# Optimization experiments

Hardware: AMD Instinct MI355X
Metric: run time of the kernel (lower is better)

## Reference

```python
import jax, jax.numpy as jnp
import numpy as np

N_NODES = 100000
N_EDGES = 640000
IN_CH = 128
OUT_CH = 64
HID = 2 * OUT_CH


def setup_inputs() -> dict:
    key = jax.random.key(0)
    k1, k2, k3, k4, k5, k6 = jax.random.split(key, 6)
    x = jax.random.normal(k1, (N_NODES, IN_CH), dtype=jnp.float32)
    edge_index = jax.random.randint(k2, (2, N_EDGES), 0, N_NODES, dtype=jnp.int64)
    # GCNConv params (PyG: glorot weights, zero bias; random values fine for a numeric reference)
    W1 = jax.random.normal(k3, (IN_CH, HID), dtype=jnp.float32) / np.sqrt(IN_CH)
    b1 = jax.random.normal(k4, (HID,), dtype=jnp.float32) * 0.01
    W2 = jax.random.normal(k5, (HID, OUT_CH), dtype=jnp.float32) / np.sqrt(HID)
    b2 = jax.random.normal(k6, (OUT_CH,), dtype=jnp.float32) * 0.01
    return {"x": x, "edge_index": edge_index, "W1": W1, "b1": b1, "W2": W2, "b2": b2}


def _gcn_conv(x, row, col, norm, W, b, n_nodes):
    # PyG GCNConv: h = x @ W; out[col] += norm * h[row]; out += b
    h = x @ W  # [N, F_out]
    msg = h[row] * norm[:, None]  # gather + scale, [E+N, F_out]
    out = jax.ops.segment_sum(msg, col, num_segments=n_nodes)  # scatter-add
    return out + b


def reference(x, edge_index, W1, b1, W2, b2):
    n_nodes = x.shape[0]
    # add self-loops (PyG default add_self_loops=True)
    loop = jnp.arange(n_nodes, dtype=edge_index.dtype)
    row = jnp.concatenate([edge_index[0], loop])  # sources
    col = jnp.concatenate([edge_index[1], loop])  # targets (aggregation index)
    # symmetric normalization: deg over targets with unit edge weights
    deg = jax.ops.segment_sum(jnp.ones_like(col, dtype=x.dtype), col, num_segments=n_nodes)
    dinv = jnp.where(deg > 0, jax.lax.rsqrt(deg), 0.0)
    norm = dinv[row] * dinv[col]  # [E+N]
    h = jax.nn.relu(_gcn_conv(x, row, col, norm, W1, b1, n_nodes))
    return _gcn_conv(h, row, col, norm, W2, b2, n_nodes)
```

## Files before the change

kernel.cpp:

```cpp
#include <hip/hip_runtime.h>

namespace {
constexpr int N_NODES = 100000;
constexpr int N_EDGES = 640000;
constexpr int ROWTILES = N_NODES / 16;
constexpr int FILLBLK = N_EDGES / 1024;
constexpr int GEMM1BLK = (ROWTILES + 3) / 4;
constexpr int UGRID = 7 * 313;
constexpr int CAP = 16;
constexpr int SPILL_CAP = 65536;
}

typedef short bf16x8 __attribute__((ext_vector_type(8)));
typedef float f32x4 __attribute__((ext_vector_type(4)));

static __device__ inline uint32_t cvt_pk_bf16(float a, float b) {
  uint32_t r;
  asm volatile("v_cvt_pk_bf16_f32 %0, %1, %2" : "=v"(r) : "v"(a), "v"(b));
  return r;
}

static __device__ inline void bf8_to_f32(uint4 u, float* v) {
  v[0] = __uint_as_float(u.x << 16);
  v[1] = __uint_as_float(u.x & 0xffff0000u);
  v[2] = __uint_as_float(u.y << 16);
  v[3] = __uint_as_float(u.y & 0xffff0000u);
  v[4] = __uint_as_float(u.z << 16);
  v[5] = __uint_as_float(u.z & 0xffff0000u);
  v[6] = __uint_as_float(u.w << 16);
  v[7] = __uint_as_float(u.w & 0xffff0000u);
}

static __device__ inline uint4 f32_to_bf8(const float* v) {
  uint4 o;
  o.x = cvt_pk_bf16(v[0], v[1]);
  o.y = cvt_pk_bf16(v[2], v[3]);
  o.z = cvt_pk_bf16(v[4], v[5]);
  o.w = cvt_pk_bf16(v[6], v[7]);
  return o;
}


static __device__ inline void wpack(const float* __restrict__ W, int kout, int idx,
                                    uint4* __restrict__ wfrag) {
  int nt_cnt = kout / 16;
  int lane = idx & 63;
  int nt = (idx >> 6) % nt_cnt;
  int ks = idx / (64 * nt_cnt);
  int g = lane >> 4, c = lane & 15;
  const float* wp = W + (ks * 32 + g * 8) * kout + nt * 16 + c;
  float w[8];
#pragma unroll
  for (int j = 0; j < 8; ++j) w[j] = wp[j * kout];
  wfrag[idx] = f32_to_bf8(w);
}

__global__ void k_wprep_zero(const float* __restrict__ W1, const float* __restrict__ W2,
                             uint4* __restrict__ wf1, uint4* __restrict__ wf2,
                             int* __restrict__ deg_zero_base) {
  int idx = blockIdx.x * 256 + threadIdx.x;
  if (idx < 2048) {
    wpack(W1, 128, idx, wf1);
  } else if (idx < 3072) {
    wpack(W2, 64, idx - 2048, wf2);
  }
  int z = idx - 3072;
  if (z >= 0 && z < N_NODES + 16) deg_zero_base[z] = 0;
}


__global__ __launch_bounds__(256) void k_histfill_gemm1(
    const int* __restrict__ erow, const int* __restrict__ ecol,
    int* __restrict__ deg, int* __restrict__ csr16, int* __restrict__ nspill,
    int2* __restrict__ spill, const float* __restrict__ X,
    const uint4* __restrict__ wfrag, unsigned short* __restrict__ Yb) {
  const int tid = threadIdx.x;
  const int group = blockIdx.x / 7;
  const int pos = blockIdx.x % 7;

  if (pos < 2) {
    const int fb = group * 2 + pos;
    if (fb >= FILLBLK) return;
    const int e4 = fb * 256 + tid;
    int4 r4 = *(const int4*)&erow[e4 * 4];
    int4 c4 = *(const int4*)&ecol[e4 * 4];
    int rs[4] = {r4.x, r4.y, r4.z, r4.w};
    int cs[4] = {c4.x, c4.y, c4.z, c4.w};
#pragma unroll
    for (int k = 0; k < 4; ++k) {
      int p = atomicAdd(&deg[cs[k]], 1);
      if (p < CAP) {
        __builtin_nontemporal_store(rs[k], &csr16[cs[k] * CAP + p]);
      } else {
        int si = atomicAdd(nspill, 1);
        if (si < SPILL_CAP) {
          __builtin_nontemporal_store(rs[k], &spill[si].x);
          __builtin_nontemporal_store(cs[k], &spill[si].y);
        }
      }
    }
    return;
  }

  const int gb = group * 5 + (pos - 2);
  if (gb >= GEMM1BLK) return;
  const int wv = gb * 4 + (tid >> 6);
  if (wv >= ROWTILES) return;
  const int lane = tid & 63;
  const int g = lane >> 4, c = lane & 15;
  const int rb = wv * 16;

  constexpr int NT = 8;
  f32x4 acc[NT];
#pragma unroll
  for (int nt = 0; nt < NT; ++nt) acc[nt] = (f32x4){0.f, 0.f, 0.f, 0.f};

  const bf16x8* wf = (const bf16x8*)wfrag;
  const float* xrow = X + (long long)(rb + c) * 128 + g * 8;

#pragma unroll
  for (int ks = 0; ks < 4; ++ks) {
    float4 a0 = *(const float4*)(xrow + ks * 32);
    float4 a1 = *(const float4*)(xrow + ks * 32 + 4);
    union { bf16x8 v; uint32_t u[4]; } af;
    af.u[0] = cvt_pk_bf16(a0.x, a0.y);
    af.u[1] = cvt_pk_bf16(a0.z, a0.w);
    af.u[2] = cvt_pk_bf16(a1.x, a1.y);
    af.u[3] = cvt_pk_bf16(a1.z, a1.w);
#pragma unroll
    for (int nt = 0; nt < NT; ++nt) {
      bf16x8 bf = wf[(ks * NT + nt) * 64 + lane];
      acc[nt] = __builtin_amdgcn_mfma_f32_16x16x32_bf16(af.v, bf, acc[nt], 0, 0, 0);
    }
  }

#pragma unroll
  for (int r = 0; r < 4; ++r) {
    int row = rb + g * 4 + r;
#pragma unroll
    for (int nt = 0; nt < NT; ++nt) {
      float val = acc[nt][r];
      Yb[(long long)row * 128 + nt * 16 + c] = (unsigned short)cvt_pk_bf16(val, val);
    }
  }
}


__global__ __launch_bounds__(128) void k_gather_gemm2(
    const int* __restrict__ deg, const int* __restrict__ csr16,
    const int* __restrict__ nspill, const int2* __restrict__ spill,
    const unsigned short* __restrict__ hs1, const float* __restrict__ b1,
    const uint4* __restrict__ wfrag2, unsigned short* __restrict__ hs2) {
  __shared__ float part[64][33];
  const int tid = threadIdx.x;
  const int wid = tid >> 6;
  const int lane = tid & 63;
  const int g = lane >> 4, c = lane & 15;
  const int rb = blockIdx.x * 16;
  const int n = rb + c;
  const int dg = deg[n];
  const int m = min(dg, CAP);
  const int base16 = n * CAP;
  const float d = rsqrtf((float)dg + 1.0f);

  float acc[4][8];
  if (wid == 0) {
    const unsigned short* hrow = hs1 + (long long)n * 128 + g * 8;
#pragma unroll
    for (int ks = 0; ks < 4; ++ks) {
      float v[8];
      bf8_to_f32(*(const uint4*)(hrow + ks * 32), v);
#pragma unroll
      for (int t = 0; t < 8; ++t) acc[ks][t] = d * v[t];
    }
  } else {
#pragma unroll
    for (int ks = 0; ks < 4; ++ks)
#pragma unroll
      for (int t = 0; t < 8; ++t) acc[ks][t] = 0.f;
  }

  int j = wid;
  for (; j + 2 < m; j += 4) {
    int s0 = csr16[base16 + j], s1 = csr16[base16 + j + 2];
    float d0 = rsqrtf((float)deg[s0] + 1.0f);
    float d1 = rsqrtf((float)deg[s1] + 1.0f);
    const unsigned short* p0 = hs1 + (long long)s0 * 128 + g * 8;
    const unsigned short* p1 = hs1 + (long long)s1 * 128 + g * 8;
#pragma unroll
    for (int ks = 0; ks < 4; ++ks) {
      float v0[8], v1[8];
      bf8_to_f32(*(const uint4*)(p0 + ks * 32), v0);
      bf8_to_f32(*(const uint4*)(p1 + ks * 32), v1);
#pragma unroll
      for (int t = 0; t < 8; ++t)
        acc[ks][t] = fmaf(d1, v1[t], fmaf(d0, v0[t], acc[ks][t]));
    }
  }
  if (j < m) {
    int s0 = csr16[base16 + j];
    float d0 = rsqrtf((float)deg[s0] + 1.0f);
    const unsigned short* p0 = hs1 + (long long)s0 * 128 + g * 8;
#pragma unroll
    for (int ks = 0; ks < 4; ++ks) {
      float v0[8];
      bf8_to_f32(*(const uint4*)(p0 + ks * 32), v0);
#pragma unroll
      for (int t = 0; t < 8; ++t) acc[ks][t] = fmaf(d0, v0[t], acc[ks][t]);
    }
  }
  if (wid == 0 && dg > CAP) {
    int ns = min(*nspill, SPILL_CAP);
    for (int i = 0; i < ns; ++i) {
      int2 p = spill[i];
      if (p.y == n) {
        float d0 = rsqrtf((float)deg[p.x] + 1.0f);
        const unsigned short* p0 = hs1 + (long long)p.x * 128 + g * 8;
#pragma unroll
        for (int ks = 0; ks < 4; ++ks) {
          float v0[8];
          bf8_to_f32(*(const uint4*)(p0 + ks * 32), v0);
#pragma unroll
          for (int t = 0; t < 8; ++t) acc[ks][t] = fmaf(d0, v0[t], acc[ks][t]);
        }
      }
    }
  }

  if (wid == 1) {
#pragma unroll
    for (int ks = 0; ks < 4; ++ks)
#pragma unroll
      for (int t = 0; t < 8; ++t) part[lane][ks * 8 + t] = acc[ks][t];
  }
  __syncthreads();
  if (wid == 1) return;
#pragma unroll
  for (int ks = 0; ks < 4; ++ks)
#pragma unroll
    for (int t = 0; t < 8; ++t) acc[ks][t] += part[lane][ks * 8 + t];

  union { bf16x8 v; uint32_t u[4]; } av[4];
#pragma unroll
  for (int ks = 0; ks < 4; ++ks) {
    float4 bv0 = *(const float4*)&b1[ks * 32 + g * 8];
    float4 bv1 = *(const float4*)&b1[ks * 32 + g * 8 + 4];
    float r8[8];
    r8[0] = fmaxf(bv0.x + d * acc[ks][0], 0.f);
    r8[1] = fmaxf(bv0.y + d * acc[ks][1], 0.f);
    r8[2] = fmaxf(bv0.z + d * acc[ks][2], 0.f);
    r8[3] = fmaxf(bv0.w + d * acc[ks][3], 0.f);
    r8[4] = fmaxf(bv1.x + d * acc[ks][4], 0.f);
    r8[5] = fmaxf(bv1.y + d * acc[ks][5], 0.f);
    r8[6] = fmaxf(bv1.z + d * acc[ks][6], 0.f);
    r8[7] = fmaxf(bv1.w + d * acc[ks][7], 0.f);
    av[ks].u[0] = cvt_pk_bf16(r8[0], r8[1]);
    av[ks].u[1] = cvt_pk_bf16(r8[2], r8[3]);
    av[ks].u[2] = cvt_pk_bf16(r8[4], r8[5]);
    av[ks].u[3] = cvt_pk_bf16(r8[6], r8[7]);
  }

  f32x4 accm[4];
#pragma unroll
  for (int nt = 0; nt < 4; ++nt) accm[nt] = (f32x4){0.f, 0.f, 0.f, 0.f};
  const bf16x8* wf = (const bf16x8*)wfrag2;
#pragma unroll
  for (int ks = 0; ks < 4; ++ks) {
#pragma unroll
    for (int nt = 0; nt < 4; ++nt) {
      bf16x8 bf = wf[(ks * 4 + nt) * 64 + lane];
      accm[nt] = __builtin_amdgcn_mfma_f32_16x16x32_bf16(av[ks].v, bf, accm[nt], 0, 0, 0);
    }
  }

#pragma unroll
  for (int r = 0; r < 4; ++r) {
    int row = rb + g * 4 + r;
    float sc = rsqrtf((float)deg[row] + 1.0f);
#pragma unroll
    for (int nt = 0; nt < 4; ++nt) {
      float val = accm[nt][r] * sc;
      hs2[(long long)row * 64 + nt * 16 + c] = (unsigned short)cvt_pk_bf16(val, val);
    }
  }
}


__global__ __launch_bounds__(256) void k_gather_out(
    const int* __restrict__ deg, const int* __restrict__ csr16,
    const int* __restrict__ nspill, const int2* __restrict__ spill,
    const unsigned short* __restrict__ hs, const float* __restrict__ bias,
    float* __restrict__ out) {
  constexpr int C = 64, Q = 8;
  int idx = blockIdx.x * 256 + threadIdx.x;
  if (idx >= N_NODES * Q) return;
  int n = idx / Q, q = idx % Q;
  int dg = deg[n];
  int m = min(dg, CAP);
  int base16 = n * CAP;
  float d = rsqrtf((float)dg + 1.0f);

  float acc[8];
  bf8_to_f32(*(const uint4*)&hs[(long long)n * C + q * 8], acc);

  int j = 0;
  for (; j + 2 <= m; j += 2) {
    int s0 = csr16[base16 + j], s1 = csr16[base16 + j + 1];
    uint4 u0 = *(const uint4*)&hs[(long long)s0 * C + q * 8];
    uint4 u1 = *(const uint4*)&hs[(long long)s1 * C + q * 8];
    float v0[8], v1[8];
    bf8_to_f32(u0, v0);
    bf8_to_f32(u1, v1);
#pragma unroll
    for (int t = 0; t < 8; ++t) acc[t] += v0[t] + v1[t];
  }
  if (j < m) {
    float v0[8];
    bf8_to_f32(*(const uint4*)&hs[(long long)csr16[base16 + j] * C + q * 8], v0);
#pragma unroll
    for (int t = 0; t < 8; ++t) acc[t] += v0[t];
  }
  if (dg > CAP) {
    int ns = min(*nspill, SPILL_CAP);
    for (int i = 0; i < ns; ++i) {
      int2 p = spill[i];
      if (p.y == n) {
        float v0[8];
        bf8_to_f32(*(const uint4*)&hs[(long long)p.x * C + q * 8], v0);
#pragma unroll
        for (int t = 0; t < 8; ++t) acc[t] += v0[t];
      }
    }
  }

  float4 bv0 = *(const float4*)&bias[q * 8];
  float4 bv1 = *(const float4*)&bias[q * 8 + 4];
  float4 o0 = {bv0.x + d * acc[0], bv0.y + d * acc[1], bv0.z + d * acc[2],
               bv0.w + d * acc[3]};
  float4 o1 = {bv1.x + d * acc[4], bv1.y + d * acc[5], bv1.z + d * acc[6],
               bv1.w + d * acc[7]};
  *(float4*)&out[(long long)n * C + q * 8] = o0;
  *(float4*)&out[(long long)n * C + q * 8 + 4] = o1;
}


extern "C" void kernel_launch(void* const* d_in, const int* in_sizes, int n_in,
                              void* d_out, int out_size, void* d_ws, size_t ws_size,
                              hipStream_t stream) {
  const float* x = (const float*)d_in[0];
  const int* ei = (const int*)d_in[1];
  const int* erow = ei;
  const int* ecol = ei + N_EDGES;
  const float* W1 = (const float*)d_in[2];
  const float* b1 = (const float*)d_in[3];
  const float* W2 = (const float*)d_in[4];
  const float* b2 = (const float*)d_in[5];
  float* out = (float*)d_out;

  char* ws = (char*)d_ws;
  int* deg = (int*)(ws + 0);
  int* nspill = (int*)(ws + 400000);
  int* csr16 = (int*)(ws + 400064);
  int2* spill = (int2*)(ws + 6800064);
  unsigned short* hs1 = (unsigned short*)(ws + 7324352);
  unsigned short* hs2 = (unsigned short*)(ws + 32924352);
  uint4* wfrag1 = (uint4*)(ws + 45724352);
  uint4* wfrag2 = (uint4*)(ws + 45757120);

  k_wprep_zero<<<(3072 + N_NODES + 16 + 255) / 256, 256, 0, stream>>>(W1, W2, wfrag1,
                                                                      wfrag2, deg);
  k_histfill_gemm1<<<UGRID, 256, 0, stream>>>(erow, ecol, deg, csr16, nspill, spill, x,
                                              wfrag1, hs1);
  k_gather_gemm2<<<ROWTILES, 128, 0, stream>>>(deg, csr16, nspill, spill, hs1, b1,
                                               wfrag2, hs2);
  k_gather_out<<<N_NODES * 8 / 256, 256, 0, stream>>>(deg, csr16, nspill, spill, hs2,
                                                      b2, out);
}
```

Baseline: 123.6 us.

## Interleave degree counter with neighbor list in one 64-byte slot per node

Merges the separate degree array and the 16-slot neighbor array into one 16-int record per node: the degree counter sits in slot 0 and up to 15 neighbors follow. Reading a node's degree and its neighbor indices then touches a single cache line rather than two arrays. Zeroing moves from the weight-prep kernel to a hipMemsetAsync over the whole 6.4 MB combined region, replacing the 400 KB zero of the old degree array. The cost is one less inline neighbor slot, so more edges go to the spill list, plus a larger memset and atomics that now land on the same lines as plain neighbor stores.

```diff
diff --git a/kernel.cpp b/kernel.cpp
--- a/kernel.cpp
+++ b/kernel.cpp
@@ -7,7 +7,7 @@
 constexpr int FILLBLK = N_EDGES / 1024;
 constexpr int GEMM1BLK = (ROWTILES + 3) / 4;
 constexpr int UGRID = 7 * 313;
-constexpr int CAP = 16;
+constexpr int CAP = 15;
 constexpr int SPILL_CAP = 65536;
 }
 
@@ -55,25 +55,22 @@
   wfrag[idx] = f32_to_bf8(w);
 }
 
-__global__ void k_wprep_zero(const float* __restrict__ W1, const float* __restrict__ W2,
-                             uint4* __restrict__ wf1, uint4* __restrict__ wf2,
-                             int* __restrict__ deg_zero_base) {
+__global__ void k_wprep(const float* __restrict__ W1, const float* __restrict__ W2,
+                        uint4* __restrict__ wf1, uint4* __restrict__ wf2) {
   int idx = blockIdx.x * 256 + threadIdx.x;
   if (idx < 2048) {
     wpack(W1, 128, idx, wf1);
   } else if (idx < 3072) {
     wpack(W2, 64, idx - 2048, wf2);
   }
-  int z = idx - 3072;
-  if (z >= 0 && z < N_NODES + 16) deg_zero_base[z] = 0;
 }
 
 
 __global__ __launch_bounds__(256) void k_histfill_gemm1(
     const int* __restrict__ erow, const int* __restrict__ ecol,
-    int* __restrict__ deg, int* __restrict__ csr16, int* __restrict__ nspill,
-    int2* __restrict__ spill, const float* __restrict__ X,
-    const uint4* __restrict__ wfrag, unsigned short* __restrict__ Yb) {
+    int* __restrict__ combined, int* __restrict__ nspill, int2* __restrict__ spill,
+    const float* __restrict__ X, const uint4* __restrict__ wfrag,
+    unsigned short* __restrict__ Yb) {
   const int tid = threadIdx.x;
   const int group = blockIdx.x / 7;
   const int pos = blockIdx.x % 7;
@@ -88,14 +85,14 @@
     int cs[4] = {c4.x, c4.y, c4.z, c4.w};
 #pragma unroll
     for (int k = 0; k < 4; ++k) {
-      int p = atomicAdd(&deg[cs[k]], 1);
+      int base = cs[k] * 16;
+      int p = atomicAdd(&combined[base], 1);
       if (p < CAP) {
-        __builtin_nontemporal_store(rs[k], &csr16[cs[k] * CAP + p]);
+        combined[base + 1 + p] = rs[k];
       } else {
         int si = atomicAdd(nspill, 1);
         if (si < SPILL_CAP) {
-          __builtin_nontemporal_store(rs[k], &spill[si].x);
-          __builtin_nontemporal_store(cs[k], &spill[si].y);
+          spill[si] = make_int2(rs[k], cs[k]);
         }
       }
     }
@@ -147,10 +144,10 @@
 
 
 __global__ __launch_bounds__(128) void k_gather_gemm2(
-    const int* __restrict__ deg, const int* __restrict__ csr16,
-    const int* __restrict__ nspill, const int2* __restrict__ spill,
-    const unsigned short* __restrict__ hs1, const float* __restrict__ b1,
-    const uint4* __restrict__ wfrag2, unsigned short* __restrict__ hs2) {
+    const int* __restrict__ combined, const int* __restrict__ nspill,
+    const int2* __restrict__ spill, const unsigned short* __restrict__ hs1,
+    const float* __restrict__ b1, const uint4* __restrict__ wfrag2,
+    unsigned short* __restrict__ hs2) {
   __shared__ float part[64][33];
   const int tid = threadIdx.x;
   const int wid = tid >> 6;
@@ -158,9 +155,9 @@
   const int g = lane >> 4, c = lane & 15;
   const int rb = blockIdx.x * 16;
   const int n = rb + c;
-  const int dg = deg[n];
+  const int nbase = n * 16;
+  const int dg = combined[nbase];
   const int m = min(dg, CAP);
-  const int base16 = n * CAP;
   const float d = rsqrtf((float)dg + 1.0f);
 
   float acc[4][8];
@@ -182,9 +179,9 @@
 
   int j = wid;
   for (; j + 2 < m; j += 4) {
-    int s0 = csr16[base16 + j], s1 = csr16[base16 + j + 2];
-    float d0 = rsqrtf((float)deg[s0] + 1.0f);
-    float d1 = rsqrtf((float)deg[s1] + 1.0f);
+    int s0 = combined[nbase + 1 + j], s1 = combined[nbase + 1 + j + 2];
+    float d0 = rsqrtf((float)combined[s0 * 16] + 1.0f);
+    float d1 = rsqrtf((float)combined[s1 * 16] + 1.0f);
     const unsigned short* p0 = hs1 + (long long)s0 * 128 + g * 8;
     const unsigned short* p1 = hs1 + (long long)s1 * 128 + g * 8;
 #pragma unroll
@@ -198,8 +195,8 @@
     }
   }
   if (j < m) {
-    int s0 = csr16[base16 + j];
-    float d0 = rsqrtf((float)deg[s0] + 1.0f);
+    int s0 = combined[nbase + 1 + j];
+    float d0 = rsqrtf((float)combined[s0 * 16] + 1.0f);
     const unsigned short* p0 = hs1 + (long long)s0 * 128 + g * 8;
 #pragma unroll
     for (int ks = 0; ks < 4; ++ks) {
@@ -214,7 +211,7 @@
     for (int i = 0; i < ns; ++i) {
       int2 p = spill[i];
       if (p.y == n) {
-        float d0 = rsqrtf((float)deg[p.x] + 1.0f);
+        float d0 = rsqrtf((float)combined[p.x * 16] + 1.0f);
         const unsigned short* p0 = hs1 + (long long)p.x * 128 + g * 8;
 #pragma unroll
         for (int ks = 0; ks < 4; ++ks) {
@@ -276,7 +273,7 @@
 #pragma unroll
   for (int r = 0; r < 4; ++r) {
     int row = rb + g * 4 + r;
-    float sc = rsqrtf((float)deg[row] + 1.0f);
+    float sc = rsqrtf((float)combined[row * 16] + 1.0f);
 #pragma unroll
     for (int nt = 0; nt < 4; ++nt) {
       float val = accm[nt][r] * sc;
@@ -287,17 +284,16 @@
 
 
 __global__ __launch_bounds__(256) void k_gather_out(
-    const int* __restrict__ deg, const int* __restrict__ csr16,
-    const int* __restrict__ nspill, const int2* __restrict__ spill,
-    const unsigned short* __restrict__ hs, const float* __restrict__ bias,
-    float* __restrict__ out) {
+    const int* __restrict__ combined, const int* __restrict__ nspill,
+    const int2* __restrict__ spill, const unsigned short* __restrict__ hs,
+    const float* __restrict__ bias, float* __restrict__ out) {
   constexpr int C = 64, Q = 8;
   int idx = blockIdx.x * 256 + threadIdx.x;
   if (idx >= N_NODES * Q) return;
   int n = idx / Q, q = idx % Q;
-  int dg = deg[n];
+  int nbase = n * 16;
+  int dg = combined[nbase];
   int m = min(dg, CAP);
-  int base16 = n * CAP;
   float d = rsqrtf((float)dg + 1.0f);
 
   float acc[8];
@@ -305,7 +301,7 @@
 
   int j = 0;
   for (; j + 2 <= m; j += 2) {
-    int s0 = csr16[base16 + j], s1 = csr16[base16 + j + 1];
+    int s0 = combined[nbase + 1 + j], s1 = combined[nbase + 1 + j + 1];
     uint4 u0 = *(const uint4*)&hs[(long long)s0 * C + q * 8];
     uint4 u1 = *(const uint4*)&hs[(long long)s1 * C + q * 8];
     float v0[8], v1[8];
@@ -316,7 +312,7 @@
   }
   if (j < m) {
     float v0[8];
-    bf8_to_f32(*(const uint4*)&hs[(long long)csr16[base16 + j] * C + q * 8], v0);
+    bf8_to_f32(*(const uint4*)&hs[(long long)combined[nbase + 1 + j] * C + q * 8], v0);
 #pragma unroll
     for (int t = 0; t < 8; ++t) acc[t] += v0[t];
   }
@@ -358,21 +354,20 @@
   float* out = (float*)d_out;
 
   char* ws = (char*)d_ws;
-  int* deg = (int*)(ws + 0);
-  int* nspill = (int*)(ws + 400000);
-  int* csr16 = (int*)(ws + 400064);
-  int2* spill = (int2*)(ws + 6800064);
-  unsigned short* hs1 = (unsigned short*)(ws + 7324352);
-  unsigned short* hs2 = (unsigned short*)(ws + 32924352);
-  uint4* wfrag1 = (uint4*)(ws + 45724352);
-  uint4* wfrag2 = (uint4*)(ws + 45757120);
-
-  k_wprep_zero<<<(3072 + N_NODES + 16 + 255) / 256, 256, 0, stream>>>(W1, W2, wfrag1,
-                                                                      wfrag2, deg);
-  k_histfill_gemm1<<<UGRID, 256, 0, stream>>>(erow, ecol, deg, csr16, nspill, spill, x,
+  int* nspill = (int*)(ws + 0);
+  int* combined = (int*)(ws + 64);
+  int2* spill = (int2*)(ws + 6400064);
+  unsigned short* hs1 = (unsigned short*)(ws + 6924352);
+  unsigned short* hs2 = (unsigned short*)(ws + 32524352);
+  uint4* wfrag1 = (uint4*)(ws + 45324352);
+  uint4* wfrag2 = (uint4*)(ws + 45357120);
+
+  hipMemsetAsync(ws, 0, 6400064, stream);
+  k_wprep<<<12, 256, 0, stream>>>(W1, W2, wfrag1, wfrag2);
+  k_histfill_gemm1<<<UGRID, 256, 0, stream>>>(erow, ecol, combined, nspill, spill, x,
                                               wfrag1, hs1);
-  k_gather_gemm2<<<ROWTILES, 128, 0, stream>>>(deg, csr16, nspill, spill, hs1, b1,
+  k_gather_gemm2<<<ROWTILES, 128, 0, stream>>>(combined, nspill, spill, hs1, b1,
                                                wfrag2, hs2);
-  k_gather_out<<<N_NODES * 8 / 256, 256, 0, stream>>>(deg, csr16, nspill, spill, hs2,
-                                                      b2, out);
-}
+  k_gather_out<<<N_NODES * 8 / 256, 256, 0, stream>>>(combined, nspill, spill, hs2, b2,
+                                                      out);
+}
```

Result: slower. 149.0 us (+20.6%).
